# Optimization experiments

Hardware: AMD Instinct MI355X
Metric: run time of the kernel (lower is better)

The kernel has to match this reference:

```python
import jax, jax.numpy as jnp
import numpy as np

N_NODES = 200000
N_EDGES = 3200000
N_GRAPHS = 4096
IN_CH = 78
H1, H2, OUT_DIM = 64, 128, 128


def setup_inputs() -> dict:
    key = jax.random.key(0)
    ks = jax.random.split(key, 10)
    x = jax.random.normal(ks[0], (N_NODES, IN_CH), dtype=jnp.float32)
    edge_index = jax.random.randint(ks[1], (2, N_EDGES), 0, N_NODES, dtype=jnp.int64)
    batch = jnp.sort(jax.random.randint(ks[2], (N_NODES,), 0, N_GRAPHS, dtype=jnp.int64))
    # GCNConv weights (PyG: lin has no bias by default; conv bias added after aggregation)
    def glorot(k, fan_in, fan_out):
        lim = jnp.sqrt(6.0 / (fan_in + fan_out)).astype(jnp.float32)
        return jax.random.uniform(k, (fan_in, fan_out), jnp.float32, -lim, lim)
    W1 = glorot(ks[3], IN_CH, H1)
    b1 = jnp.zeros((H1,), jnp.float32)
    W2 = glorot(ks[4], H1, H2)
    b2 = jnp.zeros((H2,), jnp.float32)
    fc_w = glorot(ks[5], H2, OUT_DIM)
    fc_b = jnp.zeros((OUT_DIM,), jnp.float32)
    return {"x": x, "edge_index": edge_index, "batch": batch,
            "W1": W1, "b1": b1, "W2": W2, "b2": b2, "fc_w": fc_w, "fc_b": fc_b}


def _gcn_forward(x, edge_index, batch, W1, b1, W2, b2, fc_w, fc_b):
    N = x.shape[0]
    # GCNConv default: add self loops, symmetric deg^-1/2 normalization
    self_loops = jnp.arange(N, dtype=edge_index.dtype)
    src = jnp.concatenate([edge_index[0], self_loops])  # [E+N]
    dst = jnp.concatenate([edge_index[1], self_loops])  # [E+N]
    deg = jax.ops.segment_sum(jnp.ones_like(dst, dtype=jnp.float32), dst,
                              num_segments=N)  # in-degree incl self loop
    dinv = jnp.where(deg > 0, jax.lax.rsqrt(jnp.maximum(deg, 1.0)), 0.0)
    norm = dinv[src] * dinv[dst]  # [E+N]

    def gcn_layer(h, W, b):
        hw = h @ W                              # transform first (small dims)
        msg = hw[src] * norm[:, None]           # gather + scale  [E+N, F]
        agg = jax.ops.segment_sum(msg, dst, num_segments=N)  # scatter-add
        return agg + b

    h = jax.nn.relu(gcn_layer(x, W1, b1))
    h = jax.nn.relu(gcn_layer(h, W2, b2))
    # global_mean_pool over per-graph segments
    counts = jax.ops.segment_sum(jnp.ones((N,), jnp.float32), batch,
                                 num_segments=N_GRAPHS)
    pooled = jax.ops.segment_sum(h, batch, num_segments=N_GRAPHS)
    pooled = pooled / jnp.maximum(counts, 1.0)[:, None]  # [G, H2]
    return pooled @ fc_w + fc_b                           # [G, OUT_DIM]


def reference(x, edge_index, batch, W1, b1, W2, b2, fc_w, fc_b):
    return _gcn_forward(x, edge_index, batch, W1, b1, W2, b2, fc_w, fc_b)
```

## Files before the change

### kernel.cpp

```cpp
#include <hip/hip_runtime.h>
#include <hip/hip_bf16.h>

#define NN 200000
#define NE 3200000
#define NG 4096
#define INC 78
#define C1 64
#define C2 128
#define ODIM 128
#define KP1 96

#define BSZ 256
#define NBKT 782
#define NBLK 196
#define EPB 16327
#define SCN (NBKT*NBLK)

using bf16 = __hip_bfloat16;
typedef __attribute__((ext_vector_type(8))) short bf16x8;
typedef __attribute__((ext_vector_type(4))) float f32x4;

static inline size_t alignup(size_t x) { return (x + 255) & ~size_t(255); }

__device__ __forceinline__ float bf2f(unsigned short u) {
    return __uint_as_float(((unsigned)u) << 16);
}
__device__ __forceinline__ float bflo(unsigned u) { return __uint_as_float(u << 16); }
__device__ __forceinline__ float bfhi(unsigned u) { return __uint_as_float(u & 0xffff0000u); }
__device__ __forceinline__ unsigned short f2bf(float f) {
    __hip_bfloat16 h = __float2bfloat16(f);
    return *reinterpret_cast<unsigned short*>(&h);
}

__global__ void hist1_kernel(const int* __restrict__ dst, int* __restrict__ histM) {
    __shared__ int lh[NBKT];
    for (int j = threadIdx.x; j < NBKT; j += 256) lh[j] = 0;
    __syncthreads();
    int e0 = blockIdx.x * EPB;
    int e1 = e0 + EPB; if (e1 > NE) e1 = NE;
    for (int e = e0 + threadIdx.x; e < e1; e += 256)
        atomicAdd(&lh[((unsigned)dst[e]) >> 8], 1);
    __syncthreads();
    for (int j = threadIdx.x; j < NBKT; j += 256)
        histM[j * NBLK + blockIdx.x] = lh[j];
}

__global__ void scan1_kernel(const int* __restrict__ in, int* __restrict__ out,
                             int* __restrict__ bsum, int n) {
    __shared__ int tmp[256];
    int tid = threadIdx.x, gid = blockIdx.x * 256 + tid;
    int v = (gid < n) ? in[gid] : 0;
    tmp[tid] = v;
    __syncthreads();
    for (int off = 1; off < 256; off <<= 1) {
        int t = (tid >= off) ? tmp[tid - off] : 0;
        __syncthreads();
        tmp[tid] += t;
        __syncthreads();
    }
    if (gid < n) out[gid] = tmp[tid] - v;
    if (tid == 255) bsum[blockIdx.x] = tmp[255];
}

__global__ void scan2_kernel(int* __restrict__ bsum, int nb) {
    __shared__ int tmp[1024];
    int tid = threadIdx.x;
    int v = (tid < nb) ? bsum[tid] : 0;
    tmp[tid] = v;
    __syncthreads();
    for (int off = 1; off < 1024; off <<= 1) {
        int t = (tid >= off) ? tmp[tid - off] : 0;
        __syncthreads();
        tmp[tid] += t;
        __syncthreads();
    }
    if (tid < nb) bsum[tid] = tmp[tid] - v;
}

__global__ void scan3_kernel(int* __restrict__ data, const int* __restrict__ bsum,
                             int n, int tailval) {
    int gid = blockIdx.x * 256 + threadIdx.x;
    if (gid < n) data[gid] += bsum[blockIdx.x];
    if (gid == 0) data[n] = tailval;
}

__global__ void extract_kernel(const int* __restrict__ histM, int* __restrict__ boff) {
    int j = blockIdx.x * 256 + threadIdx.x;
    if (j < NBKT) boff[j] = histM[(size_t)j * NBLK];
    if (j == NBKT) boff[NBKT] = NE;
}

__global__ void scatter2_kernel(const int* __restrict__ src, const int* __restrict__ dst,
                                const int* __restrict__ histM, unsigned* __restrict__ ebuf) {
    __shared__ int lc[NBKT];
    for (int j = threadIdx.x; j < NBKT; j += 256) lc[j] = histM[j * NBLK + blockIdx.x];
    __syncthreads();
    int e0 = blockIdx.x * EPB;
    int e1 = e0 + EPB; if (e1 > NE) e1 = NE;
    for (int e = e0 + threadIdx.x; e < e1; e += 256) {
        int d = dst[e];
        int s = src[e];
        int pos = atomicAdd(&lc[((unsigned)d) >> 8], 1);
        ebuf[pos] = ((unsigned)s << 8) | (unsigned)(d & 255);
    }
}

__global__ void deg2_kernel(const unsigned* __restrict__ ebuf, const int* __restrict__ boff,
                            int* __restrict__ degN, float* __restrict__ dinv) {
    __shared__ int cnt[BSZ];
    cnt[threadIdx.x] = 0;
    __syncthreads();
    int b = blockIdx.x;
    int s0 = boff[b], s1 = boff[b + 1];
    for (int i = s0 + threadIdx.x; i < s1; i += 256)
        atomicAdd(&cnt[ebuf[i] & 255], 1);
    __syncthreads();
    int node = b * BSZ + threadIdx.x;
    if (node < NN) {
        degN[node] = cnt[threadIdx.x];
        dinv[node] = rsqrtf((float)cnt[threadIdx.x] + 1.0f);
    }
}

__global__ void csrfill_kernel(const unsigned* __restrict__ ebuf, const int* __restrict__ boff,
                               const int* __restrict__ rs, unsigned* __restrict__ csr) {
    __shared__ int lc[BSZ];
    __shared__ int rsl[BSZ];
    int b = blockIdx.x;
    int node = b * BSZ + threadIdx.x;
    lc[threadIdx.x] = 0;
    rsl[threadIdx.x] = (node < NN) ? rs[node] : 0;
    __syncthreads();
    int s0 = boff[b], s1 = boff[b + 1];
    for (int i = s0 + threadIdx.x; i < s1; i += 256) {
        unsigned rec = ebuf[i];
        int nl = rec & 255;
        int pos = atomicAdd(&lc[nl], 1);
        csr[rsl[nl] + pos] = rec >> 8;
    }
}

__global__ void convw_kernel(const float* __restrict__ W, unsigned short* __restrict__ Wt,
                             int N, int K, int KP) {
    int idx = blockIdx.x * 256 + threadIdx.x;
    if (idx >= N * KP) return;
    int c = idx / KP, k = idx % KP;
    float f = (k < K) ? W[k * N + c] : 0.f;
    Wt[idx] = f2bf(f);
}

__global__ __launch_bounds__(256) void gemm1_mfma(const float* __restrict__ x,
                                                  const unsigned short* __restrict__ Wt1,
                                                  const float* __restrict__ dinv,
                                                  unsigned short* __restrict__ hw1s) {
    int wave = threadIdx.x >> 6, lane = threadIdx.x & 63;
    int r = lane & 15, kg = lane >> 4;
    int row0 = blockIdx.x * 64 + wave * 16;
    const float* arow = x + (size_t)(row0 + r) * INC;
    bf16x8 a[3];
    #pragma unroll
    for (int t = 0; t < 3; ++t) {
        union { bf16x8 v; unsigned short u[8]; } tmp;
        #pragma unroll
        for (int j = 0; j < 8; ++j) {
            int k = t * 32 + kg * 8 + j;
            tmp.u[j] = (k < INC) ? f2bf(arow[k]) : (unsigned short)0;
        }
        a[t] = tmp.v;
    }
    float dsc[4];
    #pragma unroll
    for (int i = 0; i < 4; ++i) dsc[i] = dinv[row0 + kg * 4 + i];
    #pragma unroll
    for (int nt = 0; nt < 4; ++nt) {
        const unsigned short* wrow = Wt1 + (size_t)(nt * 16 + r) * KP1 + kg * 8;
        bf16x8 b0 = *(const bf16x8*)(wrow);
        bf16x8 b1 = *(const bf16x8*)(wrow + 32);
        bf16x8 b2 = *(const bf16x8*)(wrow + 64);
        f32x4 acc = {0.f, 0.f, 0.f, 0.f};
        acc = __builtin_amdgcn_mfma_f32_16x16x32_bf16(a[0], b0, acc, 0, 0, 0);
        acc = __builtin_amdgcn_mfma_f32_16x16x32_bf16(a[1], b1, acc, 0, 0, 0);
        acc = __builtin_amdgcn_mfma_f32_16x16x32_bf16(a[2], b2, acc, 0, 0, 0);
        unsigned short* cb = hw1s + (size_t)(row0 + kg * 4) * C1 + nt * 16 + r;
        #pragma unroll
        for (int i = 0; i < 4; ++i) cb[(size_t)i * C1] = f2bf(acc[i] * dsc[i]);
    }
}

template <int EP>
__global__ __launch_bounds__(256) void agg_csr_kernel(
    const unsigned* __restrict__ csr, const int* __restrict__ rs,
    const float* __restrict__ dinv, const unsigned short* __restrict__ vin,
    const float* __restrict__ bias, unsigned short* __restrict__ vout) {
    int node = blockIdx.x * 16 + (threadIdx.x >> 4);
    int l = threadIdx.x & 15;
    int c0 = l * 4;
    int start = rs[node], len = rs[node + 1] - start;
    float a0 = 0.f, a1 = 0.f, a2 = 0.f, a3 = 0.f;
    int e = 0;
    for (; e + 2 <= len; e += 2) {
        unsigned sA = csr[start + e], sB = csr[start + e + 1];
        uint2 ra = *(const uint2*)(vin + (size_t)sA * 64 + c0);
        uint2 rb = *(const uint2*)(vin + (size_t)sB * 64 + c0);
        a0 += bflo(ra.x) + bflo(rb.x);
        a1 += bfhi(ra.x) + bfhi(rb.x);
        a2 += bflo(ra.y) + bflo(rb.y);
        a3 += bfhi(ra.y) + bfhi(rb.y);
    }
    if (e < len) {
        unsigned sA = csr[start + e];
        uint2 ra = *(const uint2*)(vin + (size_t)sA * 64 + c0);
        a0 += bflo(ra.x); a1 += bfhi(ra.x); a2 += bflo(ra.y); a3 += bfhi(ra.y);
    }
    uint2 sv = *(const uint2*)(vin + (size_t)node * 64 + c0);
    a0 += bflo(sv.x); a1 += bfhi(sv.x); a2 += bflo(sv.y); a3 += bfhi(sv.y);
    float d = dinv[node];
    a0 *= d; a1 *= d; a2 *= d; a3 *= d;
    if (EP == 1) {
        a0 = fmaxf(a0 + bias[c0 + 0], 0.f) * d;
        a1 = fmaxf(a1 + bias[c0 + 1], 0.f) * d;
        a2 = fmaxf(a2 + bias[c0 + 2], 0.f) * d;
        a3 = fmaxf(a3 + bias[c0 + 3], 0.f) * d;
    }
    uint2 o;
    o.x = (unsigned)f2bf(a0) | ((unsigned)f2bf(a1) << 16);
    o.y = (unsigned)f2bf(a2) | ((unsigned)f2bf(a3) << 16);
    *(uint2*)(vout + (size_t)node * 64 + c0) = o;
}

__global__ __launch_bounds__(256) void gemm2_mfma(const unsigned short* __restrict__ aggH,
                                                  const unsigned short* __restrict__ Wt2,
                                                  const float* __restrict__ b2,
                                                  unsigned short* __restrict__ h2) {
    int wave = threadIdx.x >> 6, lane = threadIdx.x & 63;
    int r = lane & 15, kg = lane >> 4;
    int row0 = blockIdx.x * 64 + wave * 16;
    const unsigned short* arow = aggH + (size_t)(row0 + r) * 64 + kg * 8;
    bf16x8 a0 = *(const bf16x8*)(arow);
    bf16x8 a1 = *(const bf16x8*)(arow + 32);
    #pragma unroll
    for (int nt = 0; nt < 8; ++nt) {
        const unsigned short* wrow = Wt2 + (size_t)(nt * 16 + r) * C1 + kg * 8;
        bf16x8 b0 = *(const bf16x8*)(wrow);
        bf16x8 b1 = *(const bf16x8*)(wrow + 32);
        f32x4 acc = {0.f, 0.f, 0.f, 0.f};
        acc = __builtin_amdgcn_mfma_f32_16x16x32_bf16(a0, b0, acc, 0, 0, 0);
        acc = __builtin_amdgcn_mfma_f32_16x16x32_bf16(a1, b1, acc, 0, 0, 0);
        int col = nt * 16 + r;
        float bb = b2[col];
        unsigned short* cb = h2 + (size_t)(row0 + kg * 4) * C2 + col;
        #pragma unroll
        for (int i = 0; i < 4; ++i) cb[(size_t)i * C2] = f2bf(fmaxf(acc[i] + bb, 0.f));
    }
}

__device__ __forceinline__ int lbound(const int* __restrict__ a, int n, int key) {
    int lo = 0, hi = n;
    while (lo < hi) {
        int mid = (lo + hi) >> 1;
        if (a[mid] < key) lo = mid + 1; else hi = mid;
    }
    return lo;
}

__global__ __launch_bounds__(256) void pool_fc_kernel(const unsigned short* __restrict__ h2,
                                                      const int* __restrict__ batch,
                                                      const float* __restrict__ fcw,
                                                      const float* __restrict__ fcb,
                                                      float* __restrict__ out) {
    __shared__ float ps[512];
    __shared__ float pr[128];
    int g = blockIdx.x;
    int lo = lbound(batch, NN, g);
    int hi = lbound(batch, NN, g + 1);
    int cnt = hi - lo;
    int rg = threadIdx.x >> 6;
    int p = threadIdx.x & 63;
    float s0 = 0.f, s1 = 0.f;
    for (int r = lo + rg; r < hi; r += 4) {
        unsigned v = *(const unsigned*)(h2 + (size_t)r * C2 + p * 2);
        s0 += bflo(v);
        s1 += bfhi(v);
    }
    ps[threadIdx.x * 2 + 0] = s0;
    ps[threadIdx.x * 2 + 1] = s1;
    __syncthreads();
    if (threadIdx.x < 64) {
        float inv = 1.0f / (float)((cnt > 0) ? cnt : 1);
        int t = threadIdx.x;
        float r0 = 0.f, r1 = 0.f;
        #pragma unroll
        for (int k = 0; k < 4; ++k) {
            r0 += ps[(k * 64 + t) * 2 + 0];
            r1 += ps[(k * 64 + t) * 2 + 1];
        }
        pr[2 * t + 0] = r0 * inv;
        pr[2 * t + 1] = r1 * inv;
    }
    __syncthreads();
    if (threadIdx.x < 128) {
        int o = threadIdx.x;
        float acc = fcb[o];
        #pragma unroll 8
        for (int k = 0; k < C2; ++k) acc += pr[k] * fcw[k * ODIM + o];
        out[(size_t)g * ODIM + o] = acc;
    }
}

extern "C" void kernel_launch(void* const* d_in, const int* in_sizes, int n_in,
                              void* d_out, int out_size, void* d_ws, size_t ws_size,
                              hipStream_t stream) {
    const float* x   = (const float*)d_in[0];
    const int*   ei  = (const int*)d_in[1];
    const int*   bat = (const int*)d_in[2];
    const float* W1  = (const float*)d_in[3];
    const float* b1  = (const float*)d_in[4];
    const float* W2  = (const float*)d_in[5];
    const float* b2  = (const float*)d_in[6];
    const float* fcw = (const float*)d_in[7];
    const float* fcb = (const float*)d_in[8];
    float* out = (float*)d_out;

    const int* src = ei;
    const int* dst = ei + NE;

    char* ws = (char*)d_ws;
    int* histM   = (int*)ws;            ws += alignup((size_t)SCN * 4);
    int* bsum    = (int*)ws;            ws += alignup(1024 * 4);
    int* boff    = (int*)ws;            ws += alignup((size_t)(NBKT + 1) * 4);
    int* degN    = (int*)ws;            ws += alignup((size_t)NN * 4);
    int* rs      = (int*)ws;            ws += alignup((size_t)(NN + 1) * 4);
    float* dinv  = (float*)ws;          ws += alignup((size_t)NN * 4);
    unsigned short* Wt1 = (unsigned short*)ws;  ws += alignup((size_t)C1 * KP1 * 2);
    unsigned short* Wt2 = (unsigned short*)ws;  ws += alignup((size_t)C2 * C1 * 2);
    unsigned short* hw1s = (unsigned short*)ws; ws += alignup((size_t)NN * C1 * 2);
    unsigned short* aggH = hw1s;
    unsigned* ebuf = (unsigned*)ws;     ws += alignup((size_t)NE * 4);
    unsigned* csr  = (unsigned*)ws;     ws += alignup((size_t)NE * 4);
    unsigned short* h1s = (unsigned short*)ws;  ws += alignup((size_t)NN * C1 * 2);
    unsigned short* h2 = (unsigned short*)ebuf;

    hist1_kernel<<<NBLK, 256, 0, stream>>>(dst, histM);
    const int SCB = (SCN + 255) / 256;
    scan1_kernel<<<SCB, 256, 0, stream>>>(histM, histM, bsum, SCN);
    scan2_kernel<<<1, 1024, 0, stream>>>(bsum, SCB);
    scan3_kernel<<<SCB, 256, 0, stream>>>(histM, bsum, SCN, 0);
    extract_kernel<<<4, 256, 0, stream>>>(histM, boff);
    scatter2_kernel<<<NBLK, 256, 0, stream>>>(src, dst, histM, ebuf);

    deg2_kernel<<<NBKT, 256, 0, stream>>>(ebuf, boff, degN, dinv);
    const int NNB = (NN + 255) / 256;
    scan1_kernel<<<NNB, 256, 0, stream>>>(degN, rs, bsum, NN);
    scan2_kernel<<<1, 1024, 0, stream>>>(bsum, NNB);
    scan3_kernel<<<NNB, 256, 0, stream>>>(rs, bsum, NN, NE);
    csrfill_kernel<<<NBKT, 256, 0, stream>>>(ebuf, boff, rs, csr);

    convw_kernel<<<(C1 * KP1 + 255) / 256, 256, 0, stream>>>(W1, Wt1, C1, INC, KP1);
    convw_kernel<<<(C2 * C1 + 255) / 256, 256, 0, stream>>>(W2, Wt2, C2, C1, C1);

    gemm1_mfma<<<NN / 64, 256, 0, stream>>>(x, Wt1, dinv, hw1s);
    agg_csr_kernel<1><<<NN / 16, 256, 0, stream>>>(csr, rs, dinv, hw1s, b1, h1s);

    agg_csr_kernel<2><<<NN / 16, 256, 0, stream>>>(csr, rs, dinv, h1s, b1, aggH);
    gemm2_mfma<<<NN / 64, 256, 0, stream>>>(aggH, Wt2, b2, h2);

    pool_fc_kernel<<<NG, 256, 0, stream>>>(h2, bat, fcw, fcb, out);
}
```

Baseline: 335.4 us.

## Fuse CSR build kernels, drop scan passes, widen aggregation loads to 16 bytes

Removes the scan3 and extract kernels by folding block sums into consumers, and fuses degree counting, the per-node scan and the CSR fill into one kernel that does a local prefix sum per bucket. It also merges the two weight-conversion launches into one. Separately, the aggregation kernel now uses 8 lanes per node with 16-byte loads and 8 accumulators, so each block covers 32 nodes. The aim is to cut launch count and per-pass global traffic and to widen the memory transactions in the gather, at the cost of more registers per thread.

```diff
diff --git a/kernel.cpp b/kernel.cpp
--- a/kernel.cpp
+++ b/kernel.cpp
@@ -22,9 +22,6 @@
 
 static inline size_t alignup(size_t x) { return (x + 255) & ~size_t(255); }
 
-__device__ __forceinline__ float bf2f(unsigned short u) {
-    return __uint_as_float(((unsigned)u) << 16);
-}
 __device__ __forceinline__ float bflo(unsigned u) { return __uint_as_float(u << 16); }
 __device__ __forceinline__ float bfhi(unsigned u) { return __uint_as_float(u & 0xffff0000u); }
 __device__ __forceinline__ unsigned short f2bf(float f) {
@@ -45,11 +42,10 @@
         histM[j * NBLK + blockIdx.x] = lh[j];
 }
 
-__global__ void scan1_kernel(const int* __restrict__ in, int* __restrict__ out,
-                             int* __restrict__ bsum, int n) {
+__global__ void scan1_kernel(int* __restrict__ data, int* __restrict__ bsum, int n) {
     __shared__ int tmp[256];
     int tid = threadIdx.x, gid = blockIdx.x * 256 + tid;
-    int v = (gid < n) ? in[gid] : 0;
+    int v = (gid < n) ? data[gid] : 0;
     tmp[tid] = v;
     __syncthreads();
     for (int off = 1; off < 256; off <<= 1) {
@@ -58,7 +54,7 @@
         tmp[tid] += t;
         __syncthreads();
     }
-    if (gid < n) out[gid] = tmp[tid] - v;
+    if (gid < n) data[gid] = tmp[tid] - v;
     if (tid == 255) bsum[blockIdx.x] = tmp[255];
 }
 
@@ -77,23 +73,14 @@
     if (tid < nb) bsum[tid] = tmp[tid] - v;
 }
 
-__global__ void scan3_kernel(int* __restrict__ data, const int* __restrict__ bsum,
-                             int n, int tailval) {
-    int gid = blockIdx.x * 256 + threadIdx.x;
-    if (gid < n) data[gid] += bsum[blockIdx.x];
-    if (gid == 0) data[n] = tailval;
-}
-
-__global__ void extract_kernel(const int* __restrict__ histM, int* __restrict__ boff) {
-    int j = blockIdx.x * 256 + threadIdx.x;
-    if (j < NBKT) boff[j] = histM[(size_t)j * NBLK];
-    if (j == NBKT) boff[NBKT] = NE;
-}
-
 __global__ void scatter2_kernel(const int* __restrict__ src, const int* __restrict__ dst,
-                                const int* __restrict__ histM, unsigned* __restrict__ ebuf) {
+                                const int* __restrict__ histM, const int* __restrict__ bsum,
+                                unsigned* __restrict__ ebuf) {
     __shared__ int lc[NBKT];
-    for (int j = threadIdx.x; j < NBKT; j += 256) lc[j] = histM[j * NBLK + blockIdx.x];
+    for (int j = threadIdx.x; j < NBKT; j += 256) {
+        int idx = j * NBLK + blockIdx.x;
+        lc[j] = histM[idx] + bsum[idx >> 8];
+    }
     __syncthreads();
     int e0 = blockIdx.x * EPB;
     int e1 = e0 + EPB; if (e1 > NE) e1 = NE;
@@ -105,48 +92,66 @@
     }
 }
 
-__global__ void deg2_kernel(const unsigned* __restrict__ ebuf, const int* __restrict__ boff,
-                            int* __restrict__ degN, float* __restrict__ dinv) {
+__global__ __launch_bounds__(256) void degcsr_kernel(
+    const unsigned* __restrict__ ebuf, const int* __restrict__ histM,
+    const int* __restrict__ bsum, int* __restrict__ rs, float* __restrict__ dinv,
+    unsigned* __restrict__ csr) {
     __shared__ int cnt[BSZ];
+    __shared__ int pfx[BSZ];
+    int b = blockIdx.x;
+    int i0 = b * NBLK;
+    int s0 = histM[i0] + bsum[i0 >> 8];
+    int s1 = NE;
+    if (b + 1 < NBKT) {
+        int i1 = (b + 1) * NBLK;
+        s1 = histM[i1] + bsum[i1 >> 8];
+    }
     cnt[threadIdx.x] = 0;
     __syncthreads();
-    int b = blockIdx.x;
-    int s0 = boff[b], s1 = boff[b + 1];
     for (int i = s0 + threadIdx.x; i < s1; i += 256)
         atomicAdd(&cnt[ebuf[i] & 255], 1);
     __syncthreads();
+    int v = cnt[threadIdx.x];
+    pfx[threadIdx.x] = v;
+    __syncthreads();
+    for (int off = 1; off < 256; off <<= 1) {
+        int t = (threadIdx.x >= off) ? pfx[threadIdx.x - off] : 0;
+        __syncthreads();
+        pfx[threadIdx.x] += t;
+        __syncthreads();
+    }
+    int myrs = s0 + pfx[threadIdx.x] - v;
     int node = b * BSZ + threadIdx.x;
     if (node < NN) {
-        degN[node] = cnt[threadIdx.x];
-        dinv[node] = rsqrtf((float)cnt[threadIdx.x] + 1.0f);
-    }
-}
-
-__global__ void csrfill_kernel(const unsigned* __restrict__ ebuf, const int* __restrict__ boff,
-                               const int* __restrict__ rs, unsigned* __restrict__ csr) {
-    __shared__ int lc[BSZ];
-    __shared__ int rsl[BSZ];
-    int b = blockIdx.x;
-    int node = b * BSZ + threadIdx.x;
-    lc[threadIdx.x] = 0;
-    rsl[threadIdx.x] = (node < NN) ? rs[node] : 0;
-    __syncthreads();
-    int s0 = boff[b], s1 = boff[b + 1];
+        rs[node] = myrs;
+        dinv[node] = rsqrtf((float)v + 1.0f);
+    }
+    if (node == NN) rs[NN] = NE;
+    __syncthreads();
+    cnt[threadIdx.x] = 0;
+    pfx[threadIdx.x] = myrs;
+    __syncthreads();
     for (int i = s0 + threadIdx.x; i < s1; i += 256) {
         unsigned rec = ebuf[i];
         int nl = rec & 255;
-        int pos = atomicAdd(&lc[nl], 1);
-        csr[rsl[nl] + pos] = rec >> 8;
-    }
-}
-
-__global__ void convw_kernel(const float* __restrict__ W, unsigned short* __restrict__ Wt,
-                             int N, int K, int KP) {
+        int pos = atomicAdd(&cnt[nl], 1);
+        csr[pfx[nl] + pos] = rec >> 8;
+    }
+}
+
+__global__ void convw2_kernel(const float* __restrict__ W1, const float* __restrict__ W2,
+                              unsigned short* __restrict__ Wt1, unsigned short* __restrict__ Wt2) {
     int idx = blockIdx.x * 256 + threadIdx.x;
-    if (idx >= N * KP) return;
-    int c = idx / KP, k = idx % KP;
-    float f = (k < K) ? W[k * N + c] : 0.f;
-    Wt[idx] = f2bf(f);
+    if (idx < C1 * KP1) {
+        int c = idx / KP1, k = idx % KP1;
+        Wt1[idx] = f2bf((k < INC) ? W1[k * C1 + c] : 0.f);
+    } else {
+        int j = idx - C1 * KP1;
+        if (j < C2 * C1) {
+            int c = j / C1, k = j % C1;
+            Wt2[j] = f2bf(W2[k * C2 + c]);
+        }
+    }
 }
 
 __global__ __launch_bounds__(256) void gemm1_mfma(const float* __restrict__ x,
@@ -192,40 +197,57 @@
     const unsigned* __restrict__ csr, const int* __restrict__ rs,
     const float* __restrict__ dinv, const unsigned short* __restrict__ vin,
     const float* __restrict__ bias, unsigned short* __restrict__ vout) {
-    int node = blockIdx.x * 16 + (threadIdx.x >> 4);
-    int l = threadIdx.x & 15;
-    int c0 = l * 4;
+    int node = blockIdx.x * 32 + (threadIdx.x >> 3);
+    int l = threadIdx.x & 7;
+    int c0 = l * 8;
     int start = rs[node], len = rs[node + 1] - start;
     float a0 = 0.f, a1 = 0.f, a2 = 0.f, a3 = 0.f;
+    float a4 = 0.f, a5 = 0.f, a6 = 0.f, a7 = 0.f;
     int e = 0;
     for (; e + 2 <= len; e += 2) {
         unsigned sA = csr[start + e], sB = csr[start + e + 1];
-        uint2 ra = *(const uint2*)(vin + (size_t)sA * 64 + c0);
-        uint2 rb = *(const uint2*)(vin + (size_t)sB * 64 + c0);
+        uint4 ra = *(const uint4*)(vin + (size_t)sA * 64 + c0);
+        uint4 rb = *(const uint4*)(vin + (size_t)sB * 64 + c0);
         a0 += bflo(ra.x) + bflo(rb.x);
         a1 += bfhi(ra.x) + bfhi(rb.x);
         a2 += bflo(ra.y) + bflo(rb.y);
         a3 += bfhi(ra.y) + bfhi(rb.y);
+        a4 += bflo(ra.z) + bflo(rb.z);
+        a5 += bfhi(ra.z) + bfhi(rb.z);
+        a6 += bflo(ra.w) + bflo(rb.w);
+        a7 += bfhi(ra.w) + bfhi(rb.w);
     }
     if (e < len) {
         unsigned sA = csr[start + e];
-        uint2 ra = *(const uint2*)(vin + (size_t)sA * 64 + c0);
-        a0 += bflo(ra.x); a1 += bfhi(ra.x); a2 += bflo(ra.y); a3 += bfhi(ra.y);
-    }
-    uint2 sv = *(const uint2*)(vin + (size_t)node * 64 + c0);
-    a0 += bflo(sv.x); a1 += bfhi(sv.x); a2 += bflo(sv.y); a3 += bfhi(sv.y);
+        uint4 ra = *(const uint4*)(vin + (size_t)sA * 64 + c0);
+        a0 += bflo(ra.x); a1 += bfhi(ra.x);
+        a2 += bflo(ra.y); a3 += bfhi(ra.y);
+        a4 += bflo(ra.z); a5 += bfhi(ra.z);
+        a6 += bflo(ra.w); a7 += bfhi(ra.w);
+    }
+    uint4 sv = *(const uint4*)(vin + (size_t)node * 64 + c0);
+    a0 += bflo(sv.x); a1 += bfhi(sv.x);
+    a2 += bflo(sv.y); a3 += bfhi(sv.y);
+    a4 += bflo(sv.z); a5 += bfhi(sv.z);
+    a6 += bflo(sv.w); a7 += bfhi(sv.w);
     float d = dinv[node];
-    a0 *= d; a1 *= d; a2 *= d; a3 *= d;
+    a0 *= d; a1 *= d; a2 *= d; a3 *= d; a4 *= d; a5 *= d; a6 *= d; a7 *= d;
     if (EP == 1) {
         a0 = fmaxf(a0 + bias[c0 + 0], 0.f) * d;
         a1 = fmaxf(a1 + bias[c0 + 1], 0.f) * d;
         a2 = fmaxf(a2 + bias[c0 + 2], 0.f) * d;
         a3 = fmaxf(a3 + bias[c0 + 3], 0.f) * d;
-    }
-    uint2 o;
+        a4 = fmaxf(a4 + bias[c0 + 4], 0.f) * d;
+        a5 = fmaxf(a5 + bias[c0 + 5], 0.f) * d;
+        a6 = fmaxf(a6 + bias[c0 + 6], 0.f) * d;
+        a7 = fmaxf(a7 + bias[c0 + 7], 0.f) * d;
+    }
+    uint4 o;
     o.x = (unsigned)f2bf(a0) | ((unsigned)f2bf(a1) << 16);
     o.y = (unsigned)f2bf(a2) | ((unsigned)f2bf(a3) << 16);
-    *(uint2*)(vout + (size_t)node * 64 + c0) = o;
+    o.z = (unsigned)f2bf(a4) | ((unsigned)f2bf(a5) << 16);
+    o.w = (unsigned)f2bf(a6) | ((unsigned)f2bf(a7) << 16);
+    *(uint4*)(vout + (size_t)node * 64 + c0) = o;
 }
 
 __global__ __launch_bounds__(256) void gemm2_mfma(const unsigned short* __restrict__ aggH,
@@ -327,8 +349,6 @@
     char* ws = (char*)d_ws;
     int* histM   = (int*)ws;            ws += alignup((size_t)SCN * 4);
     int* bsum    = (int*)ws;            ws += alignup(1024 * 4);
-    int* boff    = (int*)ws;            ws += alignup((size_t)(NBKT + 1) * 4);
-    int* degN    = (int*)ws;            ws += alignup((size_t)NN * 4);
     int* rs      = (int*)ws;            ws += alignup((size_t)(NN + 1) * 4);
     float* dinv  = (float*)ws;          ws += alignup((size_t)NN * 4);
     unsigned short* Wt1 = (unsigned short*)ws;  ws += alignup((size_t)C1 * KP1 * 2);
@@ -342,26 +362,18 @@
 
     hist1_kernel<<<NBLK, 256, 0, stream>>>(dst, histM);
     const int SCB = (SCN + 255) / 256;
-    scan1_kernel<<<SCB, 256, 0, stream>>>(histM, histM, bsum, SCN);
+    scan1_kernel<<<SCB, 256, 0, stream>>>(histM, bsum, SCN);
     scan2_kernel<<<1, 1024, 0, stream>>>(bsum, SCB);
-    scan3_kernel<<<SCB, 256, 0, stream>>>(histM, bsum, SCN, 0);
-    extract_kernel<<<4, 256, 0, stream>>>(histM, boff);
-    scatter2_kernel<<<NBLK, 256, 0, stream>>>(src, dst, histM, ebuf);
-
-    deg2_kernel<<<NBKT, 256, 0, stream>>>(ebuf, boff, degN, dinv);
-    const int NNB = (NN + 255) / 256;
-    scan1_kernel<<<NNB, 256, 0, stream>>>(degN, rs, bsum, NN);
-    scan2_kernel<<<1, 1024, 0, stream>>>(bsum, NNB);
-    scan3_kernel<<<NNB, 256, 0, stream>>>(rs, bsum, NN, NE);
-    csrfill_kernel<<<NBKT, 256, 0, stream>>>(ebuf, boff, rs, csr);
-
-    convw_kernel<<<(C1 * KP1 + 255) / 256, 256, 0, stream>>>(W1, Wt1, C1, INC, KP1);
-    convw_kernel<<<(C2 * C1 + 255) / 256, 256, 0, stream>>>(W2, Wt2, C2, C1, C1);
+    scatter2_kernel<<<NBLK, 256, 0, stream>>>(src, dst, histM, bsum, ebuf);
+
+    degcsr_kernel<<<NBKT, 256, 0, stream>>>(ebuf, histM, bsum, rs, dinv, csr);
+
+    convw2_kernel<<<(C1 * KP1 + C2 * C1 + 255) / 256, 256, 0, stream>>>(W1, W2, Wt1, Wt2);
 
     gemm1_mfma<<<NN / 64, 256, 0, stream>>>(x, Wt1, dinv, hw1s);
-    agg_csr_kernel<1><<<NN / 16, 256, 0, stream>>>(csr, rs, dinv, hw1s, b1, h1s);
-
-    agg_csr_kernel<2><<<NN / 16, 256, 0, stream>>>(csr, rs, dinv, h1s, b1, aggH);
+    agg_csr_kernel<1><<<NN / 32, 256, 0, stream>>>(csr, rs, dinv, hw1s, b1, h1s);
+
+    agg_csr_kernel<2><<<NN / 32, 256, 0, stream>>>(csr, rs, dinv, h1s, b1, aggH);
     gemm2_mfma<<<NN / 64, 256, 0, stream>>>(aggH, Wt2, b2, h2);
 
     pool_fc_kernel<<<NG, 256, 0, stream>>>(h2, bat, fcw, fcb, out);
```

After: 304.4 us. 9.2% less time.
